# Optimization experiments

Measured on AMD Instinct MI355X. Metric: run time of the kernel, lower is better.

## Reference

```python
import jax, jax.numpy as jnp
from jax import lax
import numpy as np

C = 64      # channels
K = 3       # dynamic kernel size
N = 2       # batch
H = 256
W = 256
DOWN = 4    # avgpool factor


def _conv(x, w, b):
    # 'SAME' padding matches get_same_padding for odd kernels, dilation=1
    y = lax.conv_general_dilated(x, w, (1, 1), 'SAME',
                                 dimension_numbers=('NCHW', 'OIHW', 'NCHW'))
    return y + b[None, :, None, None]


def _resblock(x, w1, b1, w2, b2):
    out = jax.nn.leaky_relu(_conv(x, w1, b1), 0.1)
    return _conv(out, w2, b2) + x


def _block(x, ws1, bs1, ws2, bs2):
    # fixed small loop over 3 structurally distinct ResBlocks
    for i in range(ws1.shape[0]):
        x = _resblock(x, ws1[i], bs1[i], ws2[i], bs2[i])
    return x


def _avgpool(x, k):
    n, c, h, w = x.shape
    return x.reshape(n, c, h // k, k, w // k, k).mean(axis=(3, 5))


def _maxpool(x, k):
    n, c, h, w = x.shape
    return x.reshape(n, c, h // k, k, w // k, k).max(axis=(3, 5))


def _dyn_conv(x, wt, k):
    # per-pixel depthwise conv: out[n,c,h,w] = sum_{dh,dw} xpad[n,c,h+dh,w+dw] * wt[n, c*k*k + dh*k + dw, h, w]
    # (torch's unfold/permute flattening pairs feat tap (dh,dw) with kernel channel index dh*k+dw)
    n, c, h, w = x.shape
    pad = (k - 1) // 2
    xp = jnp.pad(x, ((0, 0), (0, 0), (pad, pad), (pad, pad)), mode='edge')  # replicate pad
    wr = wt.reshape(n, c, k * k, h, w)
    out = jnp.zeros_like(x)
    for dh in range(k):            # fixed 3x3 tap loop; avoids materializing the unfold tensor
        for dw in range(k):
            out = out + xp[:, :, dh:dh + h, dw:dw + w] * wr[:, :, dh * k + dw]
    return out


def setup_inputs() -> dict:
    key = jax.random.key(0)
    ks = jax.random.split(key, 11)
    s = 0.05  # small init so 6 residual blocks stay numerically tame
    return {
        'x': jax.random.normal(ks[0], (N, C, H, W), jnp.float32),
        'blk1_w1': jax.random.normal(ks[1], (3, C, C, K, K), jnp.float32) * s,
        'blk1_b1': jnp.zeros((3, C), jnp.float32),
        'blk1_w2': jax.random.normal(ks[2], (3, C, C, K, K), jnp.float32) * s,
        'blk1_b2': jnp.zeros((3, C), jnp.float32),
        'blk2_w1': jax.random.normal(ks[3], (3, C, C, K, K), jnp.float32) * s,
        'blk2_b1': jnp.zeros((3, C), jnp.float32),
        'blk2_w2': jax.random.normal(ks[4], (3, C, C, K, K), jnp.float32) * s,
        'blk2_b2': jnp.zeros((3, C), jnp.float32),
        'tok_w': jax.random.normal(ks[5], (K * K * C, C, 1, 1), jnp.float32) * s,
        'tok_b': jnp.zeros((K * K * C,), jnp.float32),
    }


def reference(x, blk1_w1, blk1_b1, blk1_w2, blk1_b2,
              blk2_w1, blk2_b1, blk2_w2, blk2_b2, tok_w, tok_b):
    y = _avgpool(x, DOWN)                                   # [N,C,H/4,W/4]
    y = _block(y, blk1_w1, blk1_b1, blk1_w2, blk1_b2)
    y = _maxpool(y, 2)                                      # [N,C,H/8,W/8]
    y = _block(y, blk2_w1, blk2_b1, blk2_w2, blk2_b2)
    wt = _conv(y, tok_w, tok_b)                             # [N,9C,H/8,W/8]
    n, ck2, hs, ws = wt.shape
    # F.interpolate(scale_factor=2*down, mode='bilinear', align_corners=False)
    wt = jax.image.resize(wt, (n, ck2, hs * 2 * DOWN, ws * 2 * DOWN), method='bilinear')
    return _dyn_conv(x, wt, K)
```

## Files before the change

kernel.cpp:

```cpp
#include <hip/hip_runtime.h>


__global__ __launch_bounds__(256) void avgpool4_k(const float* __restrict__ x,
                                                  float* __restrict__ y) {
    int idx = blockIdx.x * 256 + threadIdx.x;
    int wo = idx & 63;
    int ho = (idx >> 6) & 63;
    int cz = idx >> 12;
    const float* base = x + ((long)cz * 256 + ho * 4) * 256 + wo * 4;
    float s = 0.f;
#pragma unroll
    for (int r = 0; r < 4; ++r) {
        float4 v = *(const float4*)(base + r * 256);
        s += v.x + v.y + v.z + v.w;
    }
    y[idx] = s * 0.0625f;
}

__global__ __launch_bounds__(256) void maxpool2_k(const float* __restrict__ x,
                                                  float* __restrict__ y) {
    int idx = blockIdx.x * 256 + threadIdx.x;
    int wo = idx & 31;
    int ho = (idx >> 5) & 31;
    int cz = idx >> 10;
    const float* base = x + ((long)cz * 64 + ho * 2) * 64 + wo * 2;
    float a = base[0], b = base[1], c = base[64], d = base[65];
    y[idx] = fmaxf(fmaxf(a, b), fmaxf(c, d));
}

template <int S, int OCB>
__global__ __launch_bounds__(256) void conv3x3_t(
    const float* __restrict__ in, const float* __restrict__ wgt,
    const float* __restrict__ bias, const float* __restrict__ res,
    float* __restrict__ out, int lrelu) {
    __shared__ __align__(16) float s_w[64 * 9 * OCB];
    __shared__ float s_in[16 * 342];
    const int tid = threadIdx.x;
    const int tx = tid & 15;
    const int ty = tid >> 4;
    const int tw = blockIdx.x * 16, th = blockIdx.y * 16;
    const int n = blockIdx.z / (64 / OCB);
    const int oc0 = (blockIdx.z % (64 / OCB)) * OCB;

    for (int idx = tid; idx < OCB * 576; idx += 256) {
        int k = idx / 576;
        int r = idx - k * 576;
        int ci = r / 9;
        int tap = r - ci * 9;
        s_w[(ci * 9 + tap) * OCB + k] = wgt[(long)oc0 * 576 + idx];
    }

    constexpr int NLD = 21;
    int g_off[NLD];
    int l_off[NLD];
    unsigned vmask = 0;
#pragma unroll
    for (int j = 0; j < NLD; ++j) {
        int idx = tid + j * 256;
        int t = idx < 5184 ? idx : 5183;
        int ci = t / 324;
        int rem = t - ci * 324;
        int r = rem / 18;
        int c = rem - r * 18;
        int gh = th + r - 1, gw = tw + c - 1;
        if (idx < 5184 && (unsigned)gh < (unsigned)S && (unsigned)gw < (unsigned)S)
            vmask |= (1u << j);
        int ghc = gh < 0 ? 0 : (gh > S - 1 ? S - 1 : gh);
        int gwc = gw < 0 ? 0 : (gw > S - 1 ? S - 1 : gw);
        g_off[j] = ci * S * S + ghc * S + gwc;
        l_off[j] = ci * 342 + r * 19 + c;
    }

    const float* inb = in + (long)n * 64 * S * S;
    float pf[NLD];
#pragma unroll
    for (int j = 0; j < NLD; ++j) pf[j] = inb[g_off[j]];

    float acc[OCB];
#pragma unroll
    for (int k = 0; k < OCB; ++k) acc[k] = 0.f;

    for (int chunk = 0; chunk < 64; chunk += 16) {
        __syncthreads();
#pragma unroll
        for (int j = 0; j < NLD; ++j) {
            float v = ((vmask >> j) & 1u) ? pf[j] : 0.f;
            if (j < 20 || tid < 64) s_in[l_off[j]] = v;
        }
        __syncthreads();
        if (chunk + 16 < 64) {
            const float* nb = inb + (chunk + 16) * S * S;
#pragma unroll
            for (int j = 0; j < NLD; ++j) pf[j] = nb[g_off[j]];
        }
#pragma unroll 4
        for (int ci = 0; ci < 16; ++ci) {
            const float* sp = &s_in[ci * 342 + ty * 19 + tx];
            float xw[9];
#pragma unroll
            for (int r = 0; r < 3; ++r)
#pragma unroll
                for (int c = 0; c < 3; ++c)
                    xw[r * 3 + c] = sp[r * 19 + c];
            const float* wp = &s_w[(chunk + ci) * 9 * OCB];
#pragma unroll
            for (int t = 0; t < 9; ++t) {
                float xv = xw[t];
                if constexpr (OCB == 4) {
                    float4 wv = *(const float4*)&wp[t * 4];
                    acc[0] += xv * wv.x;
                    acc[1] += xv * wv.y;
                    acc[2] += xv * wv.z;
                    acc[3] += xv * wv.w;
                } else {
                    float2 wv = *(const float2*)&wp[t * 2];
                    acc[0] += xv * wv.x;
                    acc[1] += xv * wv.y;
                }
            }
        }
    }

    const int h = th + ty, w = tw + tx;
#pragma unroll
    for (int k = 0; k < OCB; ++k) {
        int oc = oc0 + k;
        float v = acc[k] + bias[oc];
        if (lrelu) v = v > 0.f ? v : 0.1f * v;
        long off = ((long)(n * 64 + oc) * S + h) * S + w;
        if (res) v += res[off];
        out[off] = v;
    }
}

__global__ __launch_bounds__(256) void conv1x1_k(
    const float* __restrict__ in, const float* __restrict__ w,
    const float* __restrict__ b, float* __restrict__ out) {
    __shared__ float s_in[32 * 256];
    __shared__ __align__(16) float s_w[64 * 8];
    const int tid = threadIdx.x;
    const int p0 = blockIdx.x * 256;
    const int cog = blockIdx.y;
    const int n = blockIdx.z;

    for (int idx = tid; idx < 512; idx += 256) {
        int j = idx >> 6;
        int ci = idx & 63;
        s_w[ci * 8 + j] = w[(long)cog * 512 + idx];
    }

    float acc[8];
#pragma unroll
    for (int i = 0; i < 8; ++i) acc[i] = b[cog * 8 + i];

    float pf[32];
#pragma unroll
    for (int i = 0; i < 32; ++i)
        pf[i] = in[(long)(n * 64 + i) * 1024 + p0 + tid];

    for (int chunk = 0; chunk < 64; chunk += 32) {
        __syncthreads();
#pragma unroll
        for (int i = 0; i < 32; ++i) s_in[i * 256 + tid] = pf[i];
        __syncthreads();
        if (chunk + 32 < 64) {
#pragma unroll
            for (int i = 0; i < 32; ++i)
                pf[i] = in[(long)(n * 64 + chunk + 32 + i) * 1024 + p0 + tid];
        }
#pragma unroll 4
        for (int ci = 0; ci < 32; ++ci) {
            float v = s_in[ci * 256 + tid];
            float4 w0 = *(const float4*)&s_w[(chunk + ci) * 8];
            float4 w1 = *(const float4*)&s_w[(chunk + ci) * 8 + 4];
            acc[0] += v * w0.x; acc[1] += v * w0.y;
            acc[2] += v * w0.z; acc[3] += v * w0.w;
            acc[4] += v * w1.x; acc[5] += v * w1.y;
            acc[6] += v * w1.z; acc[7] += v * w1.w;
        }
    }
#pragma unroll
    for (int oc = 0; oc < 8; ++oc)
        out[(long)(n * 576 + cog * 8 + oc) * 1024 + p0 + tid] = acc[oc];
}

__global__ __launch_bounds__(256) void dynconv_k(
    const float* __restrict__ x, const float* __restrict__ wt,
    float* __restrict__ out) {
    const int w = threadIdx.x;
    const int h = blockIdx.x;
    const int cz = blockIdx.y;

    float src_h = h * 0.125f - 0.4375f;
    int h0 = (int)floorf(src_h);
    float fh = src_h - (float)h0;
    int h0c = min(max(h0, 0), 31), h1c = min(max(h0 + 1, 0), 31);
    float src_w = w * 0.125f - 0.4375f;
    int w0 = (int)floorf(src_w);
    float fw = src_w - (float)w0;
    int w0c = min(max(w0, 0), 31), w1c = min(max(w0 + 1, 0), 31);

    const float* wtb = wt + (long)cz * 9 * 1024;
    const float* xb = x + (long)cz * 65536;
    float acc = 0.f;
#pragma unroll
    for (int tap = 0; tap < 9; ++tap) {
        const float* p = wtb + tap * 1024;
        float w00 = p[h0c * 32 + w0c], w01 = p[h0c * 32 + w1c];
        float w10 = p[h1c * 32 + w0c], w11 = p[h1c * 32 + w1c];
        float top = w00 + fw * (w01 - w00);
        float bot = w10 + fw * (w11 - w10);
        float wv = top + fh * (bot - top);
        int dh = tap / 3, dw = tap - dh * 3;
        int hh = min(max(h + dh - 1, 0), 255);
        int ww = min(max(w + dw - 1, 0), 255);
        acc += xb[hh * 256 + ww] * wv;
    }
    out[(long)cz * 65536 + h * 256 + w] = acc;
}

extern "C" void kernel_launch(void* const* d_in, const int* in_sizes, int n_in,
                              void* d_out, int out_size, void* d_ws, size_t ws_size,
                              hipStream_t stream) {
    const float* x    = (const float*)d_in[0];
    const float* b1w1 = (const float*)d_in[1];
    const float* b1b1 = (const float*)d_in[2];
    const float* b1w2 = (const float*)d_in[3];
    const float* b1b2 = (const float*)d_in[4];
    const float* b2w1 = (const float*)d_in[5];
    const float* b2b1 = (const float*)d_in[6];
    const float* b2w2 = (const float*)d_in[7];
    const float* b2b2 = (const float*)d_in[8];
    const float* tokw = (const float*)d_in[9];
    const float* tokb = (const float*)d_in[10];
    float* out = (float*)d_out;
    float* ws = (float*)d_ws;

    float* A = ws;
    float* B = ws + 524288;
    float* T = ws + 1048576;
    float* P = ws;
    float* Q = ws + 131072;
    float* U = ws + 262144;
    float* WT = ws + 393216;

    const int WSZ = 64 * 64 * 9;

    avgpool4_k<<<2048, 256, 0, stream>>>(x, A);

    dim3 g64(4, 4, 32);
    conv3x3_t<64, 4><<<g64, 256, 0, stream>>>(A, b1w1 + 0 * WSZ, b1b1 + 0,   nullptr, T, 1);
    conv3x3_t<64, 4><<<g64, 256, 0, stream>>>(T, b1w2 + 0 * WSZ, b1b2 + 0,   A,       B, 0);
    conv3x3_t<64, 4><<<g64, 256, 0, stream>>>(B, b1w1 + 1 * WSZ, b1b1 + 64,  nullptr, T, 1);
    conv3x3_t<64, 4><<<g64, 256, 0, stream>>>(T, b1w2 + 1 * WSZ, b1b2 + 64,  B,       A, 0);
    conv3x3_t<64, 4><<<g64, 256, 0, stream>>>(A, b1w1 + 2 * WSZ, b1b1 + 128, nullptr, T, 1);
    conv3x3_t<64, 4><<<g64, 256, 0, stream>>>(T, b1w2 + 2 * WSZ, b1b2 + 128, A,       B, 0);

    maxpool2_k<<<512, 256, 0, stream>>>(B, P);

    dim3 g32(2, 2, 64);
    conv3x3_t<32, 2><<<g32, 256, 0, stream>>>(P, b2w1 + 0 * WSZ, b2b1 + 0,   nullptr, U, 1);
    conv3x3_t<32, 2><<<g32, 256, 0, stream>>>(U, b2w2 + 0 * WSZ, b2b2 + 0,   P,       Q, 0);
    conv3x3_t<32, 2><<<g32, 256, 0, stream>>>(Q, b2w1 + 1 * WSZ, b2b1 + 64,  nullptr, U, 1);
    conv3x3_t<32, 2><<<g32, 256, 0, stream>>>(U, b2w2 + 1 * WSZ, b2b2 + 64,  Q,       P, 0);
    conv3x3_t<32, 2><<<g32, 256, 0, stream>>>(P, b2w1 + 2 * WSZ, b2b1 + 128, nullptr, U, 1);
    conv3x3_t<32, 2><<<g32, 256, 0, stream>>>(U, b2w2 + 2 * WSZ, b2b2 + 128, P,       Q, 0);

    conv1x1_k<<<dim3(4, 72, 2), 256, 0, stream>>>(Q, tokw, tokb, WT);

    dynconv_k<<<dim3(256, 128), 256, 0, stream>>>(x, WT, out);
}
```

Measured before the change: 430.6 us.

## Tile dynamic conv with shared-memory halo and four pixels per thread

The per-pixel dynamic conv now stages a 10x130 replicate-padded input tile in LDS. Each thread computes four horizontally adjacent outputs from register-cached rows. The bilinear weight interpolation is refactored: the vertical lerp is done once per tap, then the horizontal lerp is applied per pixel, so the four scattered weight-map gathers are shared by four outputs. Output is written with float4 stores. This cuts redundant global loads and address math, at the cost of a block-wide sync and fewer, larger blocks.

Result: faster. 411.1 us (-4.5%).

```diff
diff --git a/kernel.cpp b/kernel.cpp
--- a/kernel.cpp
+++ b/kernel.cpp
@@ -187,36 +187,69 @@
 __global__ __launch_bounds__(256) void dynconv_k(
     const float* __restrict__ x, const float* __restrict__ wt,
     float* __restrict__ out) {
-    const int w = threadIdx.x;
-    const int h = blockIdx.x;
+    __shared__ __align__(16) float s_x[10 * 132];
+    const int tid = threadIdx.x;
+    const int tx = tid & 31;
+    const int ty = tid >> 5;
+    const int tw = (blockIdx.x & 1) * 128;
+    const int th = (blockIdx.x >> 1) * 8;
     const int cz = blockIdx.y;
+
+    const float* xb = x + (long)cz * 65536;
+    for (int idx = tid; idx < 1300; idx += 256) {
+        int r = idx / 130;
+        int c = idx - r * 130;
+        int gh = min(max(th + r - 1, 0), 255);
+        int gw = min(max(tw + c - 1, 0), 255);
+        s_x[r * 132 + c] = xb[gh * 256 + gw];
+    }
+
+    const int h = th + ty;
+    const int wbase = tw + tx * 4;
 
     float src_h = h * 0.125f - 0.4375f;
     int h0 = (int)floorf(src_h);
     float fh = src_h - (float)h0;
     int h0c = min(max(h0, 0), 31), h1c = min(max(h0 + 1, 0), 31);
-    float src_w = w * 0.125f - 0.4375f;
+    float src_w = wbase * 0.125f - 0.4375f;
     int w0 = (int)floorf(src_w);
-    float fw = src_w - (float)w0;
+    float fw0 = src_w - (float)w0;
     int w0c = min(max(w0, 0), 31), w1c = min(max(w0 + 1, 0), 31);
 
+    __syncthreads();
+
+    float vals[3][6];
+#pragma unroll
+    for (int r = 0; r < 3; ++r) {
+        const float* rp = &s_x[(ty + r) * 132 + tx * 4];
+        float4 a = *(const float4*)rp;
+        float2 b = *(const float2*)(rp + 4);
+        vals[r][0] = a.x; vals[r][1] = a.y; vals[r][2] = a.z;
+        vals[r][3] = a.w; vals[r][4] = b.x; vals[r][5] = b.y;
+    }
+
     const float* wtb = wt + (long)cz * 9 * 1024;
-    const float* xb = x + (long)cz * 65536;
-    float acc = 0.f;
-#pragma unroll
-    for (int tap = 0; tap < 9; ++tap) {
-        const float* p = wtb + tap * 1024;
-        float w00 = p[h0c * 32 + w0c], w01 = p[h0c * 32 + w1c];
-        float w10 = p[h1c * 32 + w0c], w11 = p[h1c * 32 + w1c];
-        float top = w00 + fw * (w01 - w00);
-        float bot = w10 + fw * (w11 - w10);
-        float wv = top + fh * (bot - top);
-        int dh = tap / 3, dw = tap - dh * 3;
-        int hh = min(max(h + dh - 1, 0), 255);
-        int ww = min(max(w + dw - 1, 0), 255);
-        acc += xb[hh * 256 + ww] * wv;
-    }
-    out[(long)cz * 65536 + h * 256 + w] = acc;
+    float acc[4] = {0.f, 0.f, 0.f, 0.f};
+#pragma unroll
+    for (int dh = 0; dh < 3; ++dh)
+#pragma unroll
+        for (int dw = 0; dw < 3; ++dw) {
+            const float* p = wtb + (dh * 3 + dw) * 1024;
+            float w00 = p[h0c * 32 + w0c], w01 = p[h0c * 32 + w1c];
+            float w10 = p[h1c * 32 + w0c], w11 = p[h1c * 32 + w1c];
+            float c0 = w00 + fh * (w10 - w00);
+            float c1 = w01 + fh * (w11 - w01);
+            float d = c1 - c0;
+#pragma unroll
+            for (int j = 0; j < 4; ++j) {
+                float wv = c0 + (fw0 + 0.125f * j) * d;
+                acc[j] += vals[dh][j + dw] * wv;
+            }
+        }
+
+    float4 o;
+    o.x = acc[0]; o.y = acc[1]; o.z = acc[2]; o.w = acc[3];
+    *(float4*)&out[(long)cz * 65536 + h * 256 + wbase] = o;
 }
 
 extern "C" void kernel_launch(void* const* d_in, const int* in_sizes, int n_in,
@@ -268,5 +301,5 @@
 
     conv1x1_k<<<dim3(4, 72, 2), 256, 0, stream>>>(Q, tokw, tokb, WT);
 
-    dynconv_k<<<dim3(256, 128), 256, 0, stream>>>(x, WT, out);
-}
+    dynconv_k<<<dim3(64, 128), 256, 0, stream>>>(x, WT, out);
+}
```
